# Optimization experiments

Hardware: AMD Instinct MI355X
Metric: run time of the kernel (lower is better)

The kernel has to match this reference:

```python
import jax, jax.numpy as jnp
import numpy as np

B, POMO, PROB, EMB, H, D = 64, 200, 200, 512, 16, 32
SQRT_EMB = 22.627416997969522  # sqrt(512)
CLIP = 10.0


def _heads(x):
    # (b, n, H*D) -> (b, H, n, D)
    b, n, _ = x.shape
    return x.reshape(b, n, H, D).transpose(0, 2, 1, 3)


def setup_inputs() -> dict:
    key = jax.random.key(0)
    ks = jax.random.split(key, 10)
    s = 1.0 / np.sqrt(EMB)
    return {
        "encoded_nodes": jax.random.normal(ks[0], (B, PROB + 1, EMB), jnp.float32),
        "encoded_q1": jax.random.normal(ks[1], (B, POMO, EMB), jnp.float32),
        "encoded_last_node": jax.random.normal(ks[2], (B, POMO, EMB), jnp.float32),
        "ninf_mask": jnp.zeros((B, POMO, PROB), jnp.float32),
        "Wq_first": jax.random.normal(ks[3], (EMB, H * D), jnp.float32) * s,
        "Wq_last": jax.random.normal(ks[4], (EMB, H * D), jnp.float32) * s,
        "Wk": jax.random.normal(ks[5], (EMB, H * D), jnp.float32) * s,
        "Wv": jax.random.normal(ks[6], (EMB, H * D), jnp.float32) * s,
        "Wc": jax.random.normal(ks[7], (H * D, EMB), jnp.float32) * s,
        "bc": jax.random.normal(ks[8], (EMB,), jnp.float32) * 0.01,
    }


def reference(encoded_nodes, encoded_q1, encoded_last_node, ninf_mask,
              Wq_first, Wq_last, Wk, Wv, Wc, bc):
    # set_kv
    k = _heads(encoded_nodes @ Wk)            # (b, H, prob+1, D)
    v = _heads(encoded_nodes @ Wv)            # (b, H, prob+1, D)
    single_head_key = encoded_nodes[:, :-1]   # (b, prob, emb)
    # set_q1 + forward queries
    q = _heads(encoded_q1 @ Wq_first) + _heads(encoded_last_node @ Wq_last)  # (b, H, pomo, D)
    # masked multi-head attention; mask padded with a zero column for the depot/last node
    mask3 = jnp.concatenate([ninf_mask, jnp.zeros((B, POMO, 1), ninf_mask.dtype)], axis=-1)
    score = jnp.einsum('bhnd,bhmd->bhnm', q, k) / jnp.sqrt(jnp.float32(D))
    weights = jax.nn.softmax(score + mask3[:, None, :, :], axis=-1)
    out = jnp.einsum('bhnm,bhmd->bhnd', weights, v)        # (b, H, pomo, D)
    out_concat = out.transpose(0, 2, 1, 3).reshape(B, POMO, H * D)
    mh_atten_out = out_concat @ Wc + bc                    # (b, pomo, emb)
    # single-head pointer score with tanh clipping
    score2 = jnp.einsum('bne,bpe->bnp', mh_atten_out, single_head_key) / SQRT_EMB
    score_masked = CLIP * jnp.tanh(score2) + ninf_mask
    return jax.nn.softmax(score_masked, axis=2)            # (b, pomo, prob)
```

## Files before the change

kernel.cpp:

```cpp
#include <hip/hip_runtime.h>
#include <cstdint>
#include <cstddef>

typedef _Float16 f16;
typedef f16 f16x4 __attribute__((ext_vector_type(4)));
typedef f16 f16x8 __attribute__((ext_vector_type(8)));
typedef float f32x4 __attribute__((ext_vector_type(4)));

#define NB    64
#define NPOMO 200
#define NNODE 201
#define NEMB  512
#define NH    16
#define ND    32

__device__ __forceinline__ void gload16(const void* g, void* l) {
  __builtin_amdgcn_global_load_lds((const __attribute__((address_space(1))) void*)g,
                                   (__attribute__((address_space(3))) void*)l, 16, 0, 0);
}


__global__ void prep_kernel(const float* __restrict__ enc, const float* __restrict__ q1,
                            const float* __restrict__ ql, const float* __restrict__ Wk,
                            const float* __restrict__ Wv, const float* __restrict__ Wqf,
                            const float* __restrict__ Wql, const float* __restrict__ Wc,
                            f16* __restrict__ Xnh, f16* __restrict__ Qcat,
                            f16* __restrict__ wkvT, f16* __restrict__ wqT,
                            f16* __restrict__ wcT) {
  const int bx = blockIdx.x;
  const int tid = threadIdx.x;
  if (bx < 6432) {
    int i = bx * 256 + tid;
    if (i < 1646592) {
      float4 v = ((const float4*)enc)[i];
      f16x4 h = {(f16)v.x, (f16)v.y, (f16)v.z, (f16)v.w};
      ((f16x4*)Xnh)[i] = h;
    }
  } else if (bx < 19232) {
    int i = (bx - 6432) * 256 + tid;
    int row = i >> 8;
    int g = i & 255;
    const float* src = (g < 128) ? (q1 + (size_t)row * 512 + g * 4)
                                 : (ql + (size_t)row * 512 + (g - 128) * 4);
    float4 v = *(const float4*)src;
    f16x4 h = {(f16)v.x, (f16)v.y, (f16)v.z, (f16)v.w};
    ((f16x4*)Qcat)[i] = h;
  } else {
    int i = (bx - 19232) * 256 + tid;
    if (i < 524288) {
      int j = i >> 9, k = i & 511;
      float v = (j < 512) ? Wk[(size_t)k * 512 + j] : Wv[(size_t)k * 512 + (j - 512)];
      wkvT[i] = (f16)v;
    } else if (i < 1048576) {
      int t = i - 524288;
      int j = t >> 10, k = t & 1023;
      float v = (k < 512) ? Wqf[(size_t)k * 512 + j] : Wql[(size_t)(k - 512) * 512 + j];
      wqT[t] = (f16)v;
    } else if (i < 1310720) {
      int t = i - 1048576;
      int j = t >> 9, k = t & 511;
      wcT[t] = (f16)Wc[(size_t)k * 512 + j];
    }
  }
}


__device__ __forceinline__ void gemm_body(
    const f16* __restrict__ A, const f16* __restrict__ B, f16* __restrict__ C,
    const float* __restrict__ bias, int M, int N, int K, int m0, int n0,
    f16* As, f16* Bs) {
  const int tid = threadIdx.x;
  const int wave = tid >> 6, lane = tid & 63;
  const int qd = lane >> 4, c = lane & 15;
  const int wm = wave >> 1, wn = wave & 1;
  const int srow = lane >> 3, sj = lane & 7;

  f32x4 acc[4][4];
#pragma unroll
  for (int i = 0; i < 4; ++i)
#pragma unroll
    for (int j = 0; j < 4; ++j) acc[i][j] = (f32x4){0.f, 0.f, 0.f, 0.f};

  for (int kc = 0; kc < K; kc += 64) {
#pragma unroll
    for (int i = 0; i < 4; ++i) {
      int row = wave * 32 + i * 8 + srow;
      int gr = m0 + row; if (gr >= M) gr = M - 1;
      int gj = sj ^ (row & 7);
      gload16(A + (size_t)gr * K + kc + gj * 8, As + row * 64 + sj * 8);
    }
#pragma unroll
    for (int i = 0; i < 4; ++i) {
      int row = wave * 32 + i * 8 + srow;
      int gj = sj ^ (row & 7);
      gload16(B + (size_t)(n0 + row) * K + kc + gj * 8, Bs + row * 64 + sj * 8);
    }
    __syncthreads();
#pragma unroll
    for (int kk = 0; kk < 2; ++kk) {
      f16x8 af[4], bf[4];
#pragma unroll
      for (int t = 0; t < 4; ++t) {
        int ra = wm * 64 + t * 16 + c;
        af[t] = *(const f16x8*)(As + ra * 64 + (((kk * 4 + qd) ^ (ra & 7)) * 8));
        int rb = wn * 64 + t * 16 + c;
        bf[t] = *(const f16x8*)(Bs + rb * 64 + (((kk * 4 + qd) ^ (rb & 7)) * 8));
      }
#pragma unroll
      for (int mt = 0; mt < 4; ++mt)
#pragma unroll
        for (int nt = 0; nt < 4; ++nt)
          acc[mt][nt] = __builtin_amdgcn_mfma_f32_16x16x32_f16(af[mt], bf[nt], acc[mt][nt], 0, 0, 0);
    }
    __syncthreads();
  }

#pragma unroll
  for (int mt = 0; mt < 4; ++mt) {
#pragma unroll
    for (int nt = 0; nt < 4; ++nt) {
      int col = n0 + wn * 64 + nt * 16 + c;
      float bv = bias ? bias[col] : 0.0f;
#pragma unroll
      for (int r = 0; r < 4; ++r) {
        int row = m0 + wm * 64 + mt * 16 + qd * 4 + r;
        if (row < M) C[(size_t)row * N + col] = (f16)(acc[mt][nt][r] + bv);
      }
    }
  }
}

__global__ __launch_bounds__(256, 2) void gemm_proj(
    const f16* __restrict__ Xnh, const f16* __restrict__ WkvT, f16* __restrict__ KVp,
    const f16* __restrict__ Qcat, const f16* __restrict__ WqT, f16* __restrict__ Qp) {
  __shared__ f16 As[128 * 64];
  __shared__ f16 Bs[128 * 64];
  const int bx = blockIdx.x;
  if (bx < 808) {
    gemm_body(Xnh, WkvT, KVp, nullptr, 12864, 1024, 512, (bx % 101) * 128, (bx / 101) * 128, As, Bs);
  } else {
    int t = bx - 808;
    gemm_body(Qcat, WqT, Qp, nullptr, 12800, 512, 1024, (t % 100) * 128, (t / 100) * 128, As, Bs);
  }
}

__global__ __launch_bounds__(256, 2) void gemm_wc(
    const f16* __restrict__ Oc, const f16* __restrict__ WcT, f16* __restrict__ mhb,
    const float* __restrict__ bc) {
  __shared__ f16 As[128 * 64];
  __shared__ f16 Bs[128 * 64];
  const int bx = blockIdx.x;
  gemm_body(Oc, WcT, mhb, bc, 12800, 512, 512, (bx % 100) * 128, (bx / 100) * 128, As, Bs);
}


#define VSTR 268

__global__ __launch_bounds__(256, 6) void attn_kernel(
    const f16* __restrict__ Qp, const f16* __restrict__ KV,
    const float* __restrict__ mask, f16* __restrict__ Oc) {
  __shared__ f16 Vt[32 * VSTR];
  const int bid = blockIdx.x;
  const int b4q = bid & 255;
  const int h = bid >> 8;
  const int b = b4q >> 2;
  const int qq = b4q & 3;
  const int tid = threadIdx.x;
  const int wave = tid >> 6, lane = tid & 63;
  const int qd = lane >> 4, c = lane & 15;

  for (int idx = tid; idx < 208 * 8; idx += 256) {
    int m = idx >> 3, ch = idx & 7;
    f16x4 v = (f16x4){0, 0, 0, 0};
    if (m < 201) v = *(const f16x4*)(KV + ((size_t)(b * NNODE + m)) * 1024 + 512 + h * 32 + ch * 4);
    Vt[(ch * 4 + 0) * VSTR + m] = v.x;
    Vt[(ch * 4 + 1) * VSTR + m] = v.y;
    Vt[(ch * 4 + 2) * VSTR + m] = v.z;
    Vt[(ch * 4 + 3) * VSTR + m] = v.w;
  }
  __syncthreads();

  const int start = (qq == 0) ? 0 : (1 + 3 * qq);
  const int ntile = (qq == 0) ? 4 : 3;
  const int rt = start + wave;
  if (wave >= ntile) return;

  const int r0 = rt * 16;
  const int qrow = min(r0 + c, 199);
  const float scale = 0.17677669529663687f;

  f16x8 aq = *(const f16x8*)(Qp + ((size_t)(b * NPOMO + qrow)) * 512 + h * 32 + qd * 8);

  f32x4 s[13];
#pragma unroll
  for (int nt = 0; nt < 13; ++nt) {
    int node = nt * 16 + c; if (node > 200) node = 200;
    f16x8 ak = *(const f16x8*)(KV + ((size_t)(b * NNODE + node)) * 1024 + h * 32 + qd * 8);
    f32x4 z = (f32x4){0.f, 0.f, 0.f, 0.f};
    s[nt] = __builtin_amdgcn_mfma_f32_16x16x32_f16(ak, aq, z, 0, 0, 0);
  }

  float mx = -3e38f;
#pragma unroll
  for (int nt = 0; nt < 13; ++nt) {
    const int col0 = nt * 16 + qd * 4;
    float4 mv = make_float4(0.f, 0.f, 0.f, 0.f);
    if (col0 < 200)
      mv = *(const float4*)(mask + ((size_t)b * NPOMO + qrow) * 200 + col0);
#pragma unroll
    for (int r = 0; r < 4; ++r) {
      int node = col0 + r;
      float v;
      if (node > 200)      v = -3e38f;
      else if (node == 200) v = s[nt][r] * scale;
      else                  v = s[nt][r] * scale + ((const float*)&mv)[r];
      s[nt][r] = v;
      mx = fmaxf(mx, v);
    }
  }
  mx = fmaxf(mx, __shfl_xor(mx, 16));
  mx = fmaxf(mx, __shfl_xor(mx, 32));

  float sm = 0.f;
  f16x4 pf[13];
#pragma unroll
  for (int nt = 0; nt < 13; ++nt) {
    f16x4 p4;
#pragma unroll
    for (int r = 0; r < 4; ++r) {
      float p = __expf(s[nt][r] - mx);
      sm += p;
      p4[r] = (f16)p;
    }
    pf[nt] = p4;
  }
  sm += __shfl_xor(sm, 16);
  sm += __shfl_xor(sm, 32);
  const float inv = 1.0f / sm;

  f32x4 o0 = (f32x4){0.f, 0.f, 0.f, 0.f};
  f32x4 o1 = (f32x4){0.f, 0.f, 0.f, 0.f};
#pragma unroll
  for (int nt = 0; nt < 13; ++nt) {
    const int nb = nt * 16 + qd * 4;
    f16x4 av0 = *(const f16x4*)(Vt + c * VSTR + nb);
    f16x4 av1 = *(const f16x4*)(Vt + (c + 16) * VSTR + nb);
    o0 = __builtin_amdgcn_mfma_f32_16x16x16f16(av0, pf[nt], o0, 0, 0, 0);
    o1 = __builtin_amdgcn_mfma_f32_16x16x16f16(av1, pf[nt], o1, 0, 0, 0);
  }

  const int row = r0 + c;
  if (row < 200) {
    f16* dst = Oc + ((size_t)(b * NPOMO + row)) * 512 + h * 32 + qd * 4;
    f16x4 w0 = {(f16)(o0[0] * inv), (f16)(o0[1] * inv), (f16)(o0[2] * inv), (f16)(o0[3] * inv)};
    f16x4 w1 = {(f16)(o1[0] * inv), (f16)(o1[1] * inv), (f16)(o1[2] * inv), (f16)(o1[3] * inv)};
    *(f16x4*)dst = w0;
    *(f16x4*)(dst + 16) = w1;
  }
}


__global__ __launch_bounds__(256, 4) void final_kernel(
    const f16* __restrict__ mh, const f16* __restrict__ Xnh,
    const float* __restrict__ mask, float* __restrict__ out) {
  __shared__ float xmax[4][16];
  __shared__ float xsum[4][16];
  const int b = blockIdx.x / 13;
  const int tile = blockIdx.x % 13;
  const int r0 = tile * 16;
  const int tid = threadIdx.x;
  const int wave = tid >> 6, lane = tid & 63;
  const int qd = lane >> 4, c = lane & 15;

  const int nt0 = (wave == 0) ? 0 : (3 * wave + 1);
  const int cnt = (wave == 0) ? 4 : 3;

  const int qrow = min(r0 + c, 199);
  const size_t rbase = ((size_t)(b * NPOMO + qrow)) * 512;

  size_t abase[4];
#pragma unroll
  for (int i = 0; i < 4; ++i) {
    int nt = nt0 + i;
    int nd = nt * 16 + c; if (nd > 200) nd = 200;
    abase[i] = ((size_t)(b * NNODE + nd)) * 512;
  }

  f32x4 acc[4];
#pragma unroll
  for (int i = 0; i < 4; ++i) acc[i] = (f32x4){0.f, 0.f, 0.f, 0.f};

#pragma unroll 4
  for (int kc = 0; kc < 512; kc += 32) {
    f16x8 bq = *(const f16x8*)(mh + rbase + kc + qd * 8);
#pragma unroll
    for (int i = 0; i < 4; ++i) {
      if (i < cnt) {
        f16x8 a = *(const f16x8*)(Xnh + abase[i] + kc + qd * 8);
        acc[i] = __builtin_amdgcn_mfma_f32_16x16x32_f16(a, bq, acc[i], 0, 0, 0);
      }
    }
  }

  const float invS = 1.0f / 22.627416997969522f;
  float mx = -3e38f;
#pragma unroll
  for (int i = 0; i < 4; ++i) {
    if (i >= cnt) break;
    const int nt = nt0 + i;
    const int col0 = nt * 16 + qd * 4;
    float4 mv = make_float4(0.f, 0.f, 0.f, 0.f);
    if (col0 < 200)
      mv = *(const float4*)(mask + ((size_t)b * NPOMO + qrow) * 200 + col0);
#pragma unroll
    for (int r = 0; r < 4; ++r) {
      int node = col0 + r;
      float v;
      if (node < 200) {
        float t = __expf(2.0f * acc[i][r] * invS);
        float th = 1.0f - 2.0f / (t + 1.0f);
        v = 10.0f * th + ((const float*)&mv)[r];
      } else {
        v = -3e38f;
      }
      acc[i][r] = v;
      mx = fmaxf(mx, v);
    }
  }
  mx = fmaxf(mx, __shfl_xor(mx, 16));
  mx = fmaxf(mx, __shfl_xor(mx, 32));
  if (lane < 16) xmax[wave][lane] = mx;
  __syncthreads();
  mx = fmaxf(fmaxf(xmax[0][c], xmax[1][c]), fmaxf(xmax[2][c], xmax[3][c]));

  float sm = 0.f;
#pragma unroll
  for (int i = 0; i < 4; ++i) {
    if (i >= cnt) break;
#pragma unroll
    for (int r = 0; r < 4; ++r) {
      float p = __expf(acc[i][r] - mx);
      acc[i][r] = p;
      sm += p;
    }
  }
  sm += __shfl_xor(sm, 16);
  sm += __shfl_xor(sm, 32);
  if (lane < 16) xsum[wave][lane] = sm;
  __syncthreads();
  const float tot = xsum[0][c] + xsum[1][c] + xsum[2][c] + xsum[3][c];
  const float inv = 1.0f / tot;

  const int row = r0 + c;
  if (row < 200) {
#pragma unroll
    for (int i = 0; i < 4; ++i) {
      if (i >= cnt) break;
      const int col0 = (nt0 + i) * 16 + qd * 4;
      if (col0 < 200) {
        float4 o;
        o.x = acc[i][0] * inv; o.y = acc[i][1] * inv;
        o.z = acc[i][2] * inv; o.w = acc[i][3] * inv;
        *(float4*)(out + ((size_t)b * NPOMO + row) * 200 + col0) = o;
      }
    }
  }
}


extern "C" void kernel_launch(void* const* d_in, const int* in_sizes, int n_in,
                              void* d_out, int out_size, void* d_ws, size_t ws_size,
                              hipStream_t stream) {
  (void)in_sizes; (void)n_in; (void)out_size; (void)ws_size;
  const float* enc   = (const float*)d_in[0];
  const float* q1    = (const float*)d_in[1];
  const float* qlast = (const float*)d_in[2];
  const float* mask  = (const float*)d_in[3];
  const float* Wqf   = (const float*)d_in[4];
  const float* Wql   = (const float*)d_in[5];
  const float* Wk    = (const float*)d_in[6];
  const float* Wv    = (const float*)d_in[7];
  const float* Wc    = (const float*)d_in[8];
  const float* bc    = (const float*)d_in[9];
  float* out = (float*)d_out;

  char* ws = (char*)d_ws;
  f16* Xnh  = (f16*)(ws + 0);
  f16* Qcat = (f16*)(ws + 13172736);
  f16* WkvT = (f16*)(ws + 39387136);
  f16* WqT  = (f16*)(ws + 40435712);
  f16* WcT  = (f16*)(ws + 41484288);
  f16* KVp  = (f16*)(ws + 42008576);
  f16* Qp   = (f16*)(ws + 68354048);
  f16* Oc   = (f16*)(ws + 81461248);
  f16* mhb  = (f16*)(ws + 94568448);

  hipLaunchKernelGGL(prep_kernel, dim3(24352), dim3(256), 0, stream,
                     enc, q1, qlast, Wk, Wv, Wqf, Wql, Wc, Xnh, Qcat, WkvT, WqT, WcT);
  hipLaunchKernelGGL(gemm_proj, dim3(1208), dim3(256), 0, stream,
                     Xnh, WkvT, KVp, Qcat, WqT, Qp);
  hipLaunchKernelGGL(attn_kernel, dim3(4096), dim3(256), 0, stream, Qp, KVp, mask, Oc);
  hipLaunchKernelGGL(gemm_wc, dim3(400), dim3(256), 0, stream, Oc, WcT, mhb, bc);
  hipLaunchKernelGGL(final_kernel, dim3(832), dim3(256), 0, stream, mhb, Xnh, mask, out);
}
```

Measured before the change: 322.1 us.

## Write V transposed from projection GEMM and drop LDS staging in attention

The K/V projection GEMM epilogue now splits its output. K goes to its own row-major buffer, and V is written directly into a per-(batch, head) transposed layout padded to 208 nodes. The attention kernel no longer transposes V into shared memory and reads the V operand straight from global memory. Each block is remapped to cover one 16-row query tile for four heads, one per wave, so no waves sit idle. The cost is scattered 2-byte stores in the GEMM epilogue, and the padding nodes 201–207 of the V buffer are never written, so uninitialized workspace values there could turn into NaN when multiplied by zero weights.

```diff
diff --git a/kernel.cpp b/kernel.cpp
--- a/kernel.cpp
+++ b/kernel.cpp
@@ -13,6 +13,7 @@
 #define NEMB  512
 #define NH    16
 #define ND    32
+#define VTSTR 208
 
 __device__ __forceinline__ void gload16(const void* g, void* l) {
   __builtin_amdgcn_global_load_lds((const __attribute__((address_space(1))) void*)g,
@@ -68,7 +69,7 @@
 __device__ __forceinline__ void gemm_body(
     const f16* __restrict__ A, const f16* __restrict__ B, f16* __restrict__ C,
     const float* __restrict__ bias, int M, int N, int K, int m0, int n0,
-    f16* As, f16* Bs) {
+    f16* As, f16* Bs, f16* __restrict__ vtp) {
   const int tid = threadIdx.x;
   const int wave = tid >> 6, lane = tid & 63;
   const int qd = lane >> 4, c = lane & 15;
@@ -124,23 +125,35 @@
 #pragma unroll
       for (int r = 0; r < 4; ++r) {
         int row = m0 + wm * 64 + mt * 16 + qd * 4 + r;
-        if (row < M) C[(size_t)row * N + col] = (f16)(acc[mt][nt][r] + bv);
+        if (row < M) {
+          f16 hv = (f16)(acc[mt][nt][r] + bv);
+          if (!vtp) {
+            C[(size_t)row * N + col] = hv;
+          } else if (col < 512) {
+            C[(size_t)row * 512 + col] = hv;
+          } else {
+            int bb = row / 201, node = row - bb * 201;
+            int hd = col - 512;
+            vtp[(((size_t)(bb * NH) + (hd >> 5)) * 32 + (hd & 31)) * VTSTR + node] = hv;
+          }
+        }
       }
     }
   }
 }
 
 __global__ __launch_bounds__(256, 2) void gemm_proj(
-    const f16* __restrict__ Xnh, const f16* __restrict__ WkvT, f16* __restrict__ KVp,
-    const f16* __restrict__ Qcat, const f16* __restrict__ WqT, f16* __restrict__ Qp) {
+    const f16* __restrict__ Xnh, const f16* __restrict__ WkvT, f16* __restrict__ Kp,
+    f16* __restrict__ VT, const f16* __restrict__ Qcat, const f16* __restrict__ WqT,
+    f16* __restrict__ Qp) {
   __shared__ f16 As[128 * 64];
   __shared__ f16 Bs[128 * 64];
   const int bx = blockIdx.x;
   if (bx < 808) {
-    gemm_body(Xnh, WkvT, KVp, nullptr, 12864, 1024, 512, (bx % 101) * 128, (bx / 101) * 128, As, Bs);
+    gemm_body(Xnh, WkvT, Kp, nullptr, 12864, 1024, 512, (bx % 101) * 128, (bx / 101) * 128, As, Bs, VT);
   } else {
     int t = bx - 808;
-    gemm_body(Qcat, WqT, Qp, nullptr, 12800, 512, 1024, (t % 100) * 128, (t / 100) * 128, As, Bs);
+    gemm_body(Qcat, WqT, Qp, nullptr, 12800, 512, 1024, (t % 100) * 128, (t / 100) * 128, As, Bs, nullptr);
   }
 }
 
@@ -150,40 +163,21 @@
   __shared__ f16 As[128 * 64];
   __shared__ f16 Bs[128 * 64];
   const int bx = blockIdx.x;
-  gemm_body(Oc, WcT, mhb, bc, 12800, 512, 512, (bx % 100) * 128, (bx / 100) * 128, As, Bs);
-}
-
-
-#define VSTR 268
-
-__global__ __launch_bounds__(256, 6) void attn_kernel(
-    const f16* __restrict__ Qp, const f16* __restrict__ KV,
-    const float* __restrict__ mask, f16* __restrict__ Oc) {
-  __shared__ f16 Vt[32 * VSTR];
+  gemm_body(Oc, WcT, mhb, bc, 12800, 512, 512, (bx % 100) * 128, (bx / 100) * 128, As, Bs, nullptr);
+}
+
+
+__global__ __launch_bounds__(256, 4) void attn_kernel(
+    const f16* __restrict__ Qp, const f16* __restrict__ Kp,
+    const f16* __restrict__ VT, const float* __restrict__ mask,
+    f16* __restrict__ Oc) {
   const int bid = blockIdx.x;
-  const int b4q = bid & 255;
-  const int h = bid >> 8;
-  const int b = b4q >> 2;
-  const int qq = b4q & 3;
-  const int tid = threadIdx.x;
-  const int wave = tid >> 6, lane = tid & 63;
+  const int hg = bid & 3;
+  const int rt = (bid >> 2) % 13;
+  const int b = bid / 52;
+  const int wave = threadIdx.x >> 6, lane = threadIdx.x & 63;
   const int qd = lane >> 4, c = lane & 15;
-
-  for (int idx = tid; idx < 208 * 8; idx += 256) {
-    int m = idx >> 3, ch = idx & 7;
-    f16x4 v = (f16x4){0, 0, 0, 0};
-    if (m < 201) v = *(const f16x4*)(KV + ((size_t)(b * NNODE + m)) * 1024 + 512 + h * 32 + ch * 4);
-    Vt[(ch * 4 + 0) * VSTR + m] = v.x;
-    Vt[(ch * 4 + 1) * VSTR + m] = v.y;
-    Vt[(ch * 4 + 2) * VSTR + m] = v.z;
-    Vt[(ch * 4 + 3) * VSTR + m] = v.w;
-  }
-  __syncthreads();
-
-  const int start = (qq == 0) ? 0 : (1 + 3 * qq);
-  const int ntile = (qq == 0) ? 4 : 3;
-  const int rt = start + wave;
-  if (wave >= ntile) return;
+  const int h = hg * 4 + wave;
 
   const int r0 = rt * 16;
   const int qrow = min(r0 + c, 199);
@@ -195,7 +189,7 @@
 #pragma unroll
   for (int nt = 0; nt < 13; ++nt) {
     int node = nt * 16 + c; if (node > 200) node = 200;
-    f16x8 ak = *(const f16x8*)(KV + ((size_t)(b * NNODE + node)) * 1024 + h * 32 + qd * 8);
+    f16x8 ak = *(const f16x8*)(Kp + ((size_t)(b * NNODE + node)) * 512 + h * 32 + qd * 8);
     f32x4 z = (f32x4){0.f, 0.f, 0.f, 0.f};
     s[nt] = __builtin_amdgcn_mfma_f32_16x16x32_f16(ak, aq, z, 0, 0, 0);
   }
@@ -238,13 +232,14 @@
   sm += __shfl_xor(sm, 32);
   const float inv = 1.0f / sm;
 
+  const f16* vbase = VT + ((size_t)(b * NH + h)) * 32 * VTSTR;
   f32x4 o0 = (f32x4){0.f, 0.f, 0.f, 0.f};
   f32x4 o1 = (f32x4){0.f, 0.f, 0.f, 0.f};
 #pragma unroll
   for (int nt = 0; nt < 13; ++nt) {
     const int nb = nt * 16 + qd * 4;
-    f16x4 av0 = *(const f16x4*)(Vt + c * VSTR + nb);
-    f16x4 av1 = *(const f16x4*)(Vt + (c + 16) * VSTR + nb);
+    f16x4 av0 = *(const f16x4*)(vbase + c * VTSTR + nb);
+    f16x4 av1 = *(const f16x4*)(vbase + (c + 16) * VTSTR + nb);
     o0 = __builtin_amdgcn_mfma_f32_16x16x16f16(av0, pf[nt], o0, 0, 0, 0);
     o1 = __builtin_amdgcn_mfma_f32_16x16x16f16(av1, pf[nt], o1, 0, 0, 0);
   }
@@ -390,16 +385,17 @@
   f16* WkvT = (f16*)(ws + 39387136);
   f16* WqT  = (f16*)(ws + 40435712);
   f16* WcT  = (f16*)(ws + 41484288);
-  f16* KVp  = (f16*)(ws + 42008576);
-  f16* Qp   = (f16*)(ws + 68354048);
-  f16* Oc   = (f16*)(ws + 81461248);
-  f16* mhb  = (f16*)(ws + 94568448);
+  f16* Kp   = (f16*)(ws + 42008576);
+  f16* VT   = (f16*)(ws + 55181312);
+  f16* Qp   = (f16*)(ws + 68812800);
+  f16* Oc   = (f16*)(ws + 81920000);
+  f16* mhb  = (f16*)(ws + 95027200);
 
   hipLaunchKernelGGL(prep_kernel, dim3(24352), dim3(256), 0, stream,
                      enc, q1, qlast, Wk, Wv, Wqf, Wql, Wc, Xnh, Qcat, WkvT, WqT, WcT);
   hipLaunchKernelGGL(gemm_proj, dim3(1208), dim3(256), 0, stream,
-                     Xnh, WkvT, KVp, Qcat, WqT, Qp);
-  hipLaunchKernelGGL(attn_kernel, dim3(4096), dim3(256), 0, stream, Qp, KVp, mask, Oc);
+                     Xnh, WkvT, Kp, VT, Qcat, WqT, Qp);
+  hipLaunchKernelGGL(attn_kernel, dim3(3328), dim3(256), 0, stream, Qp, Kp, VT, mask, Oc);
   hipLaunchKernelGGL(gemm_wc, dim3(400), dim3(256), 0, stream, Oc, WcT, mhb, bc);
   hipLaunchKernelGGL(final_kernel, dim3(832), dim3(256), 0, stream, mhb, Xnh, mask, out);
 }
```

After: 296.2 us. 1.09x faster.
